# Kernel optimization log

Hardware: AMD Instinct MI355X
Metric: run time of the kernel (lower is better)

Reference implementation:

```python
import jax, jax.numpy as jnp
import numpy as np

N = 10000
E = 160000
DIMS = [512, 512, 512, 256]  # in -> hidden -> hidden -> out (num_layers=3)
EPS = 1e-12  # F.normalize default eps


def _sage_layer(x, edge_index, Wl, b, Wr):
    # PyG SAGEConv (mean aggr, normalize=True):
    # out = lin_l(mean_{j in N(i)} x_j) + lin_r(x_i), then L2-normalize rows.
    src = edge_index[0]
    dst = edge_index[1]
    msg = x[src]  # [E, d] gather of source-node features
    agg = jax.ops.segment_sum(msg, dst, num_segments=N)  # [N, d]
    cnt = jax.ops.segment_sum(jnp.ones((E,), x.dtype), dst, num_segments=N)
    mean = agg / jnp.maximum(cnt, 1.0)[:, None]
    out = mean @ Wl.T + b + x @ Wr.T
    norm = jnp.sqrt(jnp.sum(out * out, axis=-1, keepdims=True))
    return out / jnp.maximum(norm, EPS)


def setup_inputs() -> dict:
    key = jax.random.key(0)
    ks = jax.random.split(key, 2 + 3 * len(DIMS))
    x = jax.random.normal(ks[0], (N, DIMS[0]), dtype=jnp.float32)
    edge_index = jax.random.randint(ks[1], (2, E), 0, N, dtype=jnp.int64)
    inp = {"x": x, "edge_index": edge_index}
    k = 2
    for i in range(len(DIMS) - 1):
        din, dout = DIMS[i], DIMS[i + 1]
        s = 1.0 / np.sqrt(din)
        inp[f"Wl{i}"] = jax.random.uniform(ks[k], (dout, din), jnp.float32, -s, s); k += 1
        inp[f"b{i}"] = jax.random.uniform(ks[k], (dout,), jnp.float32, -s, s); k += 1
        inp[f"Wr{i}"] = jax.random.uniform(ks[k], (dout, din), jnp.float32, -s, s); k += 1
    return inp


def reference(x, edge_index, Wl0, b0, Wr0, Wl1, b1, Wr1, Wl2, b2, Wr2):
    params = [(Wl0, b0, Wr0), (Wl1, b1, Wr1), (Wl2, b2, Wr2)]
    for Wl, b, Wr in params:
        x = _sage_layer(x, edge_index, Wl, b, Wr)
        x = jax.nn.relu(x)
        # F.dropout(training=False) is identity at inference
    return x
```

## Files before the change

kernel.cpp:

```cpp
#include <hip/hip_runtime.h>

#define NN 10000

typedef __attribute__((ext_vector_type(8))) short short8;
typedef __attribute__((ext_vector_type(4))) float f32x4;

__device__ __forceinline__ ushort f2b(float f) {
    union { float f; uint32_t u; } v; v.f = f;
    uint32_t u = v.u;
    return (ushort)((u + 0x7fffu + ((u >> 16) & 1u)) >> 16);
}
__device__ __forceinline__ uint packbf(float a, float b) {
    return (uint)f2b(a) | ((uint)f2b(b) << 16);
}
__device__ __forceinline__ float blo(uint u) {
    union { uint u; float f; } v; v.u = u << 16; return v.f;
}
__device__ __forceinline__ float bhi(uint u) {
    union { uint u; float f; } v; v.u = u & 0xffff0000u; return v.f;
}

__global__ __launch_bounds__(256) void zero_int(int* __restrict__ p, int n) {
    int i = blockIdx.x * 256 + threadIdx.x;
    if (i < n) p[i] = 0;
}

__global__ __launch_bounds__(256) void count_dst(const int* __restrict__ dst,
                                                 int* __restrict__ counts, int E) {
    int i = blockIdx.x * 256 + threadIdx.x;
    if (i < E) atomicAdd(&counts[dst[i]], 1);
}

__global__ __launch_bounds__(1024) void scan_build(const int* __restrict__ counts,
                                                   int* __restrict__ offsets,
                                                   int* __restrict__ cursor,
                                                   float* __restrict__ inv_cnt, int n) {
    __shared__ int part[1024];
    int tid = threadIdx.x;
    int per = (n + 1023) / 1024;
    int base = tid * per;
    int s = 0;
    for (int i = 0; i < per; i++) { int idx = base + i; if (idx < n) s += counts[idx]; }
    part[tid] = s;
    __syncthreads();
    for (int off = 1; off < 1024; off <<= 1) {
        int v = (tid >= off) ? part[tid - off] : 0;
        __syncthreads();
        part[tid] += v;
        __syncthreads();
    }
    int run = (tid > 0) ? part[tid - 1] : 0;
    for (int i = 0; i < per; i++) {
        int idx = base + i;
        if (idx < n) {
            int c = counts[idx];
            offsets[idx] = run;
            cursor[idx]  = run;
            inv_cnt[idx] = 1.0f / fmaxf((float)c, 1.0f);
            run += c;
        }
    }
}

__global__ __launch_bounds__(256) void scatter_edges(const int* __restrict__ src,
                                                     const int* __restrict__ dst,
                                                     int* __restrict__ cursor,
                                                     int* __restrict__ sorted_src, int E) {
    int i = blockIdx.x * 256 + threadIdx.x;
    if (i < E) {
        int p = atomicAdd(&cursor[dst[i]], 1);
        sorted_src[p] = src[i];
    }
}

__global__ __launch_bounds__(256) void cvt_x(const float* __restrict__ in,
                                             ushort* __restrict__ xcat, int n4) {
    int i = blockIdx.x * 256 + threadIdx.x;
    if (i >= n4) return;
    int idx = i * 4;
    int node = idx >> 9;
    int col  = idx & 511;
    float4 v = *(const float4*)(in + (size_t)node * 512 + col);
    uint2 p;
    p.x = packbf(v.x, v.y);
    p.y = packbf(v.z, v.w);
    *(uint2*)(xcat + (size_t)node * 1024 + 512 + col) = p;
}

__global__ __launch_bounds__(256) void cvt_w(const float* __restrict__ Wl,
                                             const float* __restrict__ Wr,
                                             ushort* __restrict__ out, int n4) {
    int i = blockIdx.x * 256 + threadIdx.x;
    if (i >= n4) return;
    int idx = i * 4;
    int row = idx >> 10;
    int col = idx & 1023;
    const float* src = (col < 512) ? (Wl + (size_t)row * 512 + col)
                                   : (Wr + (size_t)row * 512 + col - 512);
    float4 v = *(const float4*)src;
    uint2 p;
    p.x = packbf(v.x, v.y);
    p.y = packbf(v.z, v.w);
    *(uint2*)(out + idx) = p;
}

__global__ __launch_bounds__(256) void agg_mean(ushort* __restrict__ xcat,
                                                const int* __restrict__ offsets,
                                                const int* __restrict__ counts,
                                                const int* __restrict__ sorted_src,
                                                const float* __restrict__ inv_cnt, int n) {
    int wave = threadIdx.x >> 6;
    int lane = threadIdx.x & 63;
    int node = blockIdx.x * 4 + wave;
    if (node >= n) return;
    int start = offsets[node];
    int cnt   = counts[node];
    float inv = inv_cnt[node];

    const uint* xr = (const uint*)xcat + 256;
    int l4 = lane * 4;

    float acc[8];
#pragma unroll
    for (int k = 0; k < 8; k++) acc[k] = 0.f;

    int e = 0;
    for (; e + 4 <= cnt; e += 4) {
        int s0 = sorted_src[start + e + 0];
        int s1 = sorted_src[start + e + 1];
        int s2 = sorted_src[start + e + 2];
        int s3 = sorted_src[start + e + 3];
        uint4 v0 = *(const uint4*)(xr + (size_t)s0 * 512 + l4);
        uint4 v1 = *(const uint4*)(xr + (size_t)s1 * 512 + l4);
        uint4 v2 = *(const uint4*)(xr + (size_t)s2 * 512 + l4);
        uint4 v3 = *(const uint4*)(xr + (size_t)s3 * 512 + l4);
#define ACC8(v) do { \
        acc[0] += blo(v.x); acc[1] += bhi(v.x); \
        acc[2] += blo(v.y); acc[3] += bhi(v.y); \
        acc[4] += blo(v.z); acc[5] += bhi(v.z); \
        acc[6] += blo(v.w); acc[7] += bhi(v.w); } while (0)
        ACC8(v0); ACC8(v1); ACC8(v2); ACC8(v3);
    }
    for (; e < cnt; e++) {
        int s0 = sorted_src[start + e];
        uint4 v0 = *(const uint4*)(xr + (size_t)s0 * 512 + l4);
        ACC8(v0);
    }
#undef ACC8

    uint4 o;
    o.x = packbf(acc[0] * inv, acc[1] * inv);
    o.y = packbf(acc[2] * inv, acc[3] * inv);
    o.z = packbf(acc[4] * inv, acc[5] * inv);
    o.w = packbf(acc[6] * inv, acc[7] * inv);
    *(uint4*)(xcat + (size_t)node * 1024 + lane * 8) = o;
}

__global__ __launch_bounds__(256) void gemm_mfma(const ushort* __restrict__ A,
                                                 const ushort* __restrict__ B,
                                                 float* __restrict__ C,
                                                 int M, int Nn) {
    __shared__ ushort Asl[64 * 32];
    __shared__ ushort Bsl[128 * 32];
    const int tid  = threadIdx.x;
    const int w    = tid >> 6;
    const int lane = tid & 63;
    const int bm = blockIdx.y * 64, bn = blockIdx.x * 128;
    const int wm = (w & 1) * 32, wn = (w >> 1) * 64;
    const int row16 = lane & 15, q = lane >> 4;

    f32x4 acc[2][4];
#pragma unroll
    for (int i = 0; i < 2; i++)
#pragma unroll
        for (int j = 0; j < 4; j++) acc[i][j] = (f32x4){0.f, 0.f, 0.f, 0.f};

    const int sc_r = lane >> 2;
    const int sc_s = lane & 3;
    const int koff = sc_s ^ ((sc_r >> 1) & 3);
    const int swz  = (row16 >> 1) & 3;

    for (int k0 = 0; k0 < 1024; k0 += 32) {
        {
            int rloc = w * 16 + sc_r;
            int grow = bm + rloc; grow = grow < M ? grow : M - 1;
            const ushort* gp = A + (size_t)grow * 1024 + k0 + koff * 8;
            __builtin_amdgcn_global_load_lds(
                (const __attribute__((address_space(1))) uint32_t*)gp,
                (__attribute__((address_space(3))) uint32_t*)&Asl[w * 512],
                16, 0, 0);
        }
#pragma unroll
        for (int c = 0; c < 2; c++) {
            int chunk = w * 2 + c;
            int rloc  = chunk * 16 + sc_r;
            const ushort* gp = B + (size_t)(bn + rloc) * 1024 + k0 + koff * 8;
            __builtin_amdgcn_global_load_lds(
                (const __attribute__((address_space(1))) uint32_t*)gp,
                (__attribute__((address_space(3))) uint32_t*)&Bsl[chunk * 512],
                16, 0, 0);
        }
        __syncthreads();

        short8 af[2], bfr[4];
        int s = q ^ swz;
#pragma unroll
        for (int i = 0; i < 2; i++) {
            int r = wm + i * 16 + row16;
            af[i] = *(const short8*)&Asl[r * 32 + s * 8];
        }
#pragma unroll
        for (int j = 0; j < 4; j++) {
            int rn = wn + j * 16 + row16;
            bfr[j] = *(const short8*)&Bsl[rn * 32 + s * 8];
        }
#pragma unroll
        for (int i = 0; i < 2; i++)
#pragma unroll
            for (int j = 0; j < 4; j++)
                acc[i][j] = __builtin_amdgcn_mfma_f32_16x16x32_bf16(
                    af[i], bfr[j], acc[i][j], 0, 0, 0);
        __syncthreads();
    }

#pragma unroll
    for (int i = 0; i < 2; i++) {
#pragma unroll
        for (int r2 = 0; r2 < 4; r2++) {
            int row = bm + wm + i * 16 + q * 4 + r2;
            if (row < M) {
                float* Cp = C + (size_t)row * Nn + bn + wn + row16;
#pragma unroll
                for (int j = 0; j < 4; j++)
                    Cp[j * 16] = acc[i][j][r2];
            }
        }
    }
}

template <int DOUT, bool FINAL>
__global__ __launch_bounds__(256) void finalize(const float* __restrict__ Cbuf,
                                                const float* __restrict__ bias,
                                                ushort* __restrict__ xcat,
                                                float* __restrict__ outf, int n) {
    const int PL = DOUT / 64;
    int wave = threadIdx.x >> 6;
    int lane = threadIdx.x & 63;
    int node = blockIdx.x * 4 + wave;
    if (node >= n) return;

    float v[PL];
    const float* Cp = Cbuf + (size_t)node * DOUT + lane * PL;
    const float* Bp = bias + lane * PL;
#pragma unroll
    for (int k = 0; k < PL; k += 4) {
        float4 c = *(const float4*)(Cp + k);
        float4 b = *(const float4*)(Bp + k);
        v[k + 0] = c.x + b.x; v[k + 1] = c.y + b.y;
        v[k + 2] = c.z + b.z; v[k + 3] = c.w + b.w;
    }
    float ss = 0.f;
#pragma unroll
    for (int k = 0; k < PL; k++) ss += v[k] * v[k];
#pragma unroll
    for (int m = 32; m >= 1; m >>= 1) ss += __shfl_xor(ss, m, 64);
    float scale = 1.0f / fmaxf(sqrtf(ss), 1e-12f);

    if (FINAL) {
        float* Op = outf + (size_t)node * DOUT + lane * PL;
#pragma unroll
        for (int k = 0; k < PL; k += 4) {
            float4 o;
            o.x = fmaxf(v[k + 0] * scale, 0.f);
            o.y = fmaxf(v[k + 1] * scale, 0.f);
            o.z = fmaxf(v[k + 2] * scale, 0.f);
            o.w = fmaxf(v[k + 3] * scale, 0.f);
            *(float4*)(Op + k) = o;
        }
    } else {
        uint4 o;
        float r0 = fmaxf(v[0] * scale, 0.f), r1 = fmaxf(v[1] * scale, 0.f);
        float r2 = fmaxf(v[2] * scale, 0.f), r3 = fmaxf(v[3] * scale, 0.f);
        float r4 = fmaxf(v[4] * scale, 0.f), r5 = fmaxf(v[5] * scale, 0.f);
        float r6 = fmaxf(v[6] * scale, 0.f), r7 = fmaxf(v[7] * scale, 0.f);
        o.x = packbf(r0, r1); o.y = packbf(r2, r3);
        o.z = packbf(r4, r5); o.w = packbf(r6, r7);
        *(uint4*)(xcat + (size_t)node * 1024 + 512 + lane * 8) = o;
    }
}

extern "C" void kernel_launch(void* const* d_in, const int* in_sizes, int n_in,
                              void* d_out, int out_size, void* d_ws, size_t ws_size,
                              hipStream_t stream) {
    const float* x    = (const float*)d_in[0];
    const int*   edge = (const int*)d_in[1];
    const float* Wl0  = (const float*)d_in[2];
    const float* b0   = (const float*)d_in[3];
    const float* Wr0  = (const float*)d_in[4];
    const float* Wl1  = (const float*)d_in[5];
    const float* b1   = (const float*)d_in[6];
    const float* Wr1  = (const float*)d_in[7];
    const float* Wl2  = (const float*)d_in[8];
    const float* b2   = (const float*)d_in[9];
    const float* Wr2  = (const float*)d_in[10];

    const int E = in_sizes[1] / 2;

    char* ws = (char*)d_ws;
    int*    counts  = (int*)(ws + 0);
    int*    offsets = (int*)(ws + 40960);
    int*    cursor  = (int*)(ws + 81920);
    float*  invc    = (float*)(ws + 122880);
    int*    sorted  = (int*)(ws + 163840);
    ushort* Wc0     = (ushort*)(ws + 804864);
    ushort* Wc1     = (ushort*)(ws + 1853440);
    ushort* Wc2     = (ushort*)(ws + 2902016);
    ushort* xcat    = (ushort*)(ws + 3426304);
    float*  Cbuf    = (float*)(ws + 23906304);

    zero_int<<<(NN + 255) / 256, 256, 0, stream>>>(counts, NN);
    count_dst<<<(E + 255) / 256, 256, 0, stream>>>(edge + E, counts, E);
    scan_build<<<1, 1024, 0, stream>>>(counts, offsets, cursor, invc, NN);
    scatter_edges<<<(E + 255) / 256, 256, 0, stream>>>(edge, edge + E, cursor, sorted, E);

    cvt_x<<<(NN * 512 / 4 + 255) / 256, 256, 0, stream>>>(x, xcat, NN * 512 / 4);
    cvt_w<<<(512 * 1024 / 4 + 255) / 256, 256, 0, stream>>>(Wl0, Wr0, Wc0, 512 * 1024 / 4);
    cvt_w<<<(512 * 1024 / 4 + 255) / 256, 256, 0, stream>>>(Wl1, Wr1, Wc1, 512 * 1024 / 4);
    cvt_w<<<(256 * 1024 / 4 + 255) / 256, 256, 0, stream>>>(Wl2, Wr2, Wc2, 256 * 1024 / 4);

    const int gyM = (NN + 63) / 64;
    const int gb  = (NN + 3) / 4;

    agg_mean<<<gb, 256, 0, stream>>>(xcat, offsets, counts, sorted, invc, NN);
    gemm_mfma<<<dim3(4, gyM), 256, 0, stream>>>(xcat, Wc0, Cbuf, NN, 512);
    finalize<512, false><<<gb, 256, 0, stream>>>(Cbuf, b0, xcat, nullptr, NN);
    agg_mean<<<gb, 256, 0, stream>>>(xcat, offsets, counts, sorted, invc, NN);
    gemm_mfma<<<dim3(4, gyM), 256, 0, stream>>>(xcat, Wc1, Cbuf, NN, 512);
    finalize<512, false><<<gb, 256, 0, stream>>>(Cbuf, b1, xcat, nullptr, NN);
    agg_mean<<<gb, 256, 0, stream>>>(xcat, offsets, counts, sorted, invc, NN);
    gemm_mfma<<<dim3(2, gyM), 256, 0, stream>>>(xcat, Wc2, Cbuf, NN, 256);
    finalize<256, true><<<gb, 256, 0, stream>>>(Cbuf, b2, nullptr, (float*)d_out, NN);
}
```

Measured before the change: 276.6 us.

## Fuse bias and row sum-of-squares into GEMM epilogue, store bf16 output

The GEMM epilogue now adds the bias, writes the result as bf16 instead of fp32, and accumulates each row's sum of squares into a buffer with a shuffle reduction plus atomicAdd. The old finalize kernel becomes a light apply_scale pass that only reads bf16 and the precomputed norm. This halves intermediate traffic and removes the per-row reduction pass. Other changes: agg_mean zeroes that buffer and unrolls its gather loop to 8 edges for more loads in flight, and the three weight-conversion launches are merged into one. The cost is rounding before normalization and float atomics, which make the reduction order nondeterministic.

```diff
diff --git a/kernel.cpp b/kernel.cpp
--- a/kernel.cpp
+++ b/kernel.cpp
@@ -87,16 +87,24 @@
     *(uint2*)(xcat + (size_t)node * 1024 + 512 + col) = p;
 }
 
-__global__ __launch_bounds__(256) void cvt_w(const float* __restrict__ Wl,
-                                             const float* __restrict__ Wr,
-                                             ushort* __restrict__ out, int n4) {
+__global__ __launch_bounds__(256) void cvt_w_all(const float* __restrict__ Wl0,
+                                                 const float* __restrict__ Wr0,
+                                                 const float* __restrict__ Wl1,
+                                                 const float* __restrict__ Wr1,
+                                                 const float* __restrict__ Wl2,
+                                                 const float* __restrict__ Wr2,
+                                                 ushort* __restrict__ out, int n4) {
     int i = blockIdx.x * 256 + threadIdx.x;
     if (i >= n4) return;
     int idx = i * 4;
     int row = idx >> 10;
     int col = idx & 1023;
-    const float* src = (col < 512) ? (Wl + (size_t)row * 512 + col)
-                                   : (Wr + (size_t)row * 512 + col - 512);
+    const float* Wl; const float* Wr; int r;
+    if (row < 512)       { Wl = Wl0; Wr = Wr0; r = row; }
+    else if (row < 1024) { Wl = Wl1; Wr = Wr1; r = row - 512; }
+    else                 { Wl = Wl2; Wr = Wr2; r = row - 1024; }
+    const float* src = (col < 512) ? (Wl + (size_t)r * 512 + col)
+                                   : (Wr + (size_t)r * 512 + col - 512);
     float4 v = *(const float4*)src;
     uint2 p;
     p.x = packbf(v.x, v.y);
@@ -108,7 +116,12 @@
                                                 const int* __restrict__ offsets,
                                                 const int* __restrict__ counts,
                                                 const int* __restrict__ sorted_src,
-                                                const float* __restrict__ inv_cnt, int n) {
+                                                const float* __restrict__ inv_cnt,
+                                                float* __restrict__ rowss, int n) {
+    if (threadIdx.x < 16) {
+        int z = blockIdx.x * 16 + (int)threadIdx.x;
+        if (z < n) rowss[z] = 0.f;
+    }
     int wave = threadIdx.x >> 6;
     int lane = threadIdx.x & 63;
     int node = blockIdx.x * 4 + wave;
@@ -124,22 +137,22 @@
 #pragma unroll
     for (int k = 0; k < 8; k++) acc[k] = 0.f;
 
+#define ACC8(v) do { \
+    acc[0] += blo(v.x); acc[1] += bhi(v.x); \
+    acc[2] += blo(v.y); acc[3] += bhi(v.y); \
+    acc[4] += blo(v.z); acc[5] += bhi(v.z); \
+    acc[6] += blo(v.w); acc[7] += bhi(v.w); } while (0)
+
     int e = 0;
-    for (; e + 4 <= cnt; e += 4) {
-        int s0 = sorted_src[start + e + 0];
-        int s1 = sorted_src[start + e + 1];
-        int s2 = sorted_src[start + e + 2];
-        int s3 = sorted_src[start + e + 3];
-        uint4 v0 = *(const uint4*)(xr + (size_t)s0 * 512 + l4);
-        uint4 v1 = *(const uint4*)(xr + (size_t)s1 * 512 + l4);
-        uint4 v2 = *(const uint4*)(xr + (size_t)s2 * 512 + l4);
-        uint4 v3 = *(const uint4*)(xr + (size_t)s3 * 512 + l4);
-#define ACC8(v) do { \
-        acc[0] += blo(v.x); acc[1] += bhi(v.x); \
-        acc[2] += blo(v.y); acc[3] += bhi(v.y); \
-        acc[4] += blo(v.z); acc[5] += bhi(v.z); \
-        acc[6] += blo(v.w); acc[7] += bhi(v.w); } while (0)
-        ACC8(v0); ACC8(v1); ACC8(v2); ACC8(v3);
+    for (; e + 8 <= cnt; e += 8) {
+        int s[8];
+#pragma unroll
+        for (int u = 0; u < 8; u++) s[u] = sorted_src[start + e + u];
+        uint4 v[8];
+#pragma unroll
+        for (int u = 0; u < 8; u++) v[u] = *(const uint4*)(xr + (size_t)s[u] * 512 + l4);
+#pragma unroll
+        for (int u = 0; u < 8; u++) ACC8(v[u]);
     }
     for (; e < cnt; e++) {
         int s0 = sorted_src[start + e];
@@ -158,7 +171,9 @@
 
 __global__ __launch_bounds__(256) void gemm_mfma(const ushort* __restrict__ A,
                                                  const ushort* __restrict__ B,
-                                                 float* __restrict__ C,
+                                                 const float* __restrict__ bias,
+                                                 ushort* __restrict__ Cb,
+                                                 float* __restrict__ rowss,
                                                  int M, int Nn) {
     __shared__ ushort Asl[64 * 32];
     __shared__ ushort Bsl[128 * 32];
@@ -223,69 +238,65 @@
         __syncthreads();
     }
 
+    float bias_v[4];
+#pragma unroll
+    for (int j = 0; j < 4; j++) bias_v[j] = bias[bn + wn + row16 + j * 16];
+
 #pragma unroll
     for (int i = 0; i < 2; i++) {
 #pragma unroll
         for (int r2 = 0; r2 < 4; r2++) {
             int row = bm + wm + i * 16 + q * 4 + r2;
+            float v0 = acc[i][0][r2] + bias_v[0];
+            float v1 = acc[i][1][r2] + bias_v[1];
+            float v2 = acc[i][2][r2] + bias_v[2];
+            float v3 = acc[i][3][r2] + bias_v[3];
+            float ssp = v0 * v0 + v1 * v1 + v2 * v2 + v3 * v3;
+            ssp += __shfl_xor(ssp, 1, 64);
+            ssp += __shfl_xor(ssp, 2, 64);
+            ssp += __shfl_xor(ssp, 4, 64);
+            ssp += __shfl_xor(ssp, 8, 64);
             if (row < M) {
-                float* Cp = C + (size_t)row * Nn + bn + wn + row16;
-#pragma unroll
-                for (int j = 0; j < 4; j++)
-                    Cp[j * 16] = acc[i][j][r2];
+                ushort* Cp = Cb + (size_t)row * Nn + bn + wn + row16;
+                Cp[0]  = f2b(v0);
+                Cp[16] = f2b(v1);
+                Cp[32] = f2b(v2);
+                Cp[48] = f2b(v3);
+                if (row16 == 0) atomicAdd(&rowss[row], ssp);
             }
         }
     }
 }
 
 template <int DOUT, bool FINAL>
-__global__ __launch_bounds__(256) void finalize(const float* __restrict__ Cbuf,
-                                                const float* __restrict__ bias,
-                                                ushort* __restrict__ xcat,
-                                                float* __restrict__ outf, int n) {
-    const int PL = DOUT / 64;
+__global__ __launch_bounds__(256) void apply_scale(const ushort* __restrict__ Cb,
+                                                   const float* __restrict__ rowss,
+                                                   ushort* __restrict__ xcat,
+                                                   float* __restrict__ outf, int n) {
     int wave = threadIdx.x >> 6;
     int lane = threadIdx.x & 63;
     int node = blockIdx.x * 4 + wave;
     if (node >= n) return;
-
-    float v[PL];
-    const float* Cp = Cbuf + (size_t)node * DOUT + lane * PL;
-    const float* Bp = bias + lane * PL;
-#pragma unroll
-    for (int k = 0; k < PL; k += 4) {
-        float4 c = *(const float4*)(Cp + k);
-        float4 b = *(const float4*)(Bp + k);
-        v[k + 0] = c.x + b.x; v[k + 1] = c.y + b.y;
-        v[k + 2] = c.z + b.z; v[k + 3] = c.w + b.w;
-    }
-    float ss = 0.f;
-#pragma unroll
-    for (int k = 0; k < PL; k++) ss += v[k] * v[k];
-#pragma unroll
-    for (int m = 32; m >= 1; m >>= 1) ss += __shfl_xor(ss, m, 64);
-    float scale = 1.0f / fmaxf(sqrtf(ss), 1e-12f);
-
-    if (FINAL) {
-        float* Op = outf + (size_t)node * DOUT + lane * PL;
-#pragma unroll
-        for (int k = 0; k < PL; k += 4) {
-            float4 o;
-            o.x = fmaxf(v[k + 0] * scale, 0.f);
-            o.y = fmaxf(v[k + 1] * scale, 0.f);
-            o.z = fmaxf(v[k + 2] * scale, 0.f);
-            o.w = fmaxf(v[k + 3] * scale, 0.f);
-            *(float4*)(Op + k) = o;
-        }
-    } else {
+    float scale = 1.0f / fmaxf(sqrtf(rowss[node]), 1e-12f);
+
+    if (DOUT == 512) {
+        uint4 v = *(const uint4*)(Cb + (size_t)node * 512 + lane * 8);
+        float r0 = fmaxf(blo(v.x) * scale, 0.f), r1 = fmaxf(bhi(v.x) * scale, 0.f);
+        float r2 = fmaxf(blo(v.y) * scale, 0.f), r3 = fmaxf(bhi(v.y) * scale, 0.f);
+        float r4 = fmaxf(blo(v.z) * scale, 0.f), r5 = fmaxf(bhi(v.z) * scale, 0.f);
+        float r6 = fmaxf(blo(v.w) * scale, 0.f), r7 = fmaxf(bhi(v.w) * scale, 0.f);
         uint4 o;
-        float r0 = fmaxf(v[0] * scale, 0.f), r1 = fmaxf(v[1] * scale, 0.f);
-        float r2 = fmaxf(v[2] * scale, 0.f), r3 = fmaxf(v[3] * scale, 0.f);
-        float r4 = fmaxf(v[4] * scale, 0.f), r5 = fmaxf(v[5] * scale, 0.f);
-        float r6 = fmaxf(v[6] * scale, 0.f), r7 = fmaxf(v[7] * scale, 0.f);
         o.x = packbf(r0, r1); o.y = packbf(r2, r3);
         o.z = packbf(r4, r5); o.w = packbf(r6, r7);
         *(uint4*)(xcat + (size_t)node * 1024 + 512 + lane * 8) = o;
+    } else {
+        uint2 v = *(const uint2*)(Cb + (size_t)node * 256 + lane * 4);
+        float4 o;
+        o.x = fmaxf(blo(v.x) * scale, 0.f);
+        o.y = fmaxf(bhi(v.x) * scale, 0.f);
+        o.z = fmaxf(blo(v.y) * scale, 0.f);
+        o.w = fmaxf(bhi(v.y) * scale, 0.f);
+        *(float4*)(outf + (size_t)node * 256 + lane * 4) = o;
     }
 }
 
@@ -312,11 +323,14 @@
     int*    cursor  = (int*)(ws + 81920);
     float*  invc    = (float*)(ws + 122880);
     int*    sorted  = (int*)(ws + 163840);
-    ushort* Wc0     = (ushort*)(ws + 804864);
-    ushort* Wc1     = (ushort*)(ws + 1853440);
-    ushort* Wc2     = (ushort*)(ws + 2902016);
+    ushort* Wcat    = (ushort*)(ws + 804864);
     ushort* xcat    = (ushort*)(ws + 3426304);
-    float*  Cbuf    = (float*)(ws + 23906304);
+    ushort* Cb      = (ushort*)(ws + 23906304);
+    float*  rowss   = (float*)(ws + 34146304);
+
+    ushort* Wc0 = Wcat;
+    ushort* Wc1 = Wcat + 512 * 1024;
+    ushort* Wc2 = Wcat + 1024 * 1024;
 
     zero_int<<<(NN + 255) / 256, 256, 0, stream>>>(counts, NN);
     count_dst<<<(E + 255) / 256, 256, 0, stream>>>(edge + E, counts, E);
@@ -324,20 +338,19 @@
     scatter_edges<<<(E + 255) / 256, 256, 0, stream>>>(edge, edge + E, cursor, sorted, E);
 
     cvt_x<<<(NN * 512 / 4 + 255) / 256, 256, 0, stream>>>(x, xcat, NN * 512 / 4);
-    cvt_w<<<(512 * 1024 / 4 + 255) / 256, 256, 0, stream>>>(Wl0, Wr0, Wc0, 512 * 1024 / 4);
-    cvt_w<<<(512 * 1024 / 4 + 255) / 256, 256, 0, stream>>>(Wl1, Wr1, Wc1, 512 * 1024 / 4);
-    cvt_w<<<(256 * 1024 / 4 + 255) / 256, 256, 0, stream>>>(Wl2, Wr2, Wc2, 256 * 1024 / 4);
+    cvt_w_all<<<(1280 * 1024 / 4 + 255) / 256, 256, 0, stream>>>(
+        Wl0, Wr0, Wl1, Wr1, Wl2, Wr2, Wcat, 1280 * 1024 / 4);
 
     const int gyM = (NN + 63) / 64;
     const int gb  = (NN + 3) / 4;
 
-    agg_mean<<<gb, 256, 0, stream>>>(xcat, offsets, counts, sorted, invc, NN);
-    gemm_mfma<<<dim3(4, gyM), 256, 0, stream>>>(xcat, Wc0, Cbuf, NN, 512);
-    finalize<512, false><<<gb, 256, 0, stream>>>(Cbuf, b0, xcat, nullptr, NN);
-    agg_mean<<<gb, 256, 0, stream>>>(xcat, offsets, counts, sorted, invc, NN);
-    gemm_mfma<<<dim3(4, gyM), 256, 0, stream>>>(xcat, Wc1, Cbuf, NN, 512);
-    finalize<512, false><<<gb, 256, 0, stream>>>(Cbuf, b1, xcat, nullptr, NN);
-    agg_mean<<<gb, 256, 0, stream>>>(xcat, offsets, counts, sorted, invc, NN);
-    gemm_mfma<<<dim3(2, gyM), 256, 0, stream>>>(xcat, Wc2, Cbuf, NN, 256);
-    finalize<256, true><<<gb, 256, 0, stream>>>(Cbuf, b2, nullptr, (float*)d_out, NN);
-}
+    agg_mean<<<gb, 256, 0, stream>>>(xcat, offsets, counts, sorted, invc, rowss, NN);
+    gemm_mfma<<<dim3(4, gyM), 256, 0, stream>>>(xcat, Wc0, b0, Cb, rowss, NN, 512);
+    apply_scale<512, false><<<gb, 256, 0, stream>>>(Cb, rowss, xcat, nullptr, NN);
+    agg_mean<<<gb, 256, 0, stream>>>(xcat, offsets, counts, sorted, invc, rowss, NN);
+    gemm_mfma<<<dim3(4, gyM), 256, 0, stream>>>(xcat, Wc1, b1, Cb, rowss, NN, 512);
+    apply_scale<512, false><<<gb, 256, 0, stream>>>(Cb, rowss, xcat, nullptr, NN);
+    agg_mean<<<gb, 256, 0, stream>>>(xcat, offsets, counts, sorted, invc, rowss, NN);
+    gemm_mfma<<<dim3(2, gyM), 256, 0, stream>>>(xcat, Wc2, b2, Cb, rowss, NN, 256);
+    apply_scale<256, true><<<gb, 256, 0, stream>>>(Cb, rowss, nullptr, (float*)d_out, NN);
+}
```

New measurement: 280.5 us. Within noise of the previous version (+1.4%).

## Shard neighbor aggregation by feature chunk and fuse setup kernels

Applied to the files above, without the earlier changes.

The mean aggregation now splits each node's 512 features into 8 chunks handled by separate blocks, with 16 lanes per node and 8 edges unrolled per step. The aim is more memory-level parallelism and a smaller per-block gather footprint, so that chunked neighbor rows may stay resident in cache. Separately, count zeroing is folded into cvt_x, edge counting into a single merged weight-conversion kernel, and the three weight conversions are merged into one launch to cut launch overhead. The risks are narrower 8-byte gathers, and that counting inside cvt_w_all depends on cvt_x having zeroed counts earlier on the same stream.

```diff
diff --git a/kernel.cpp b/kernel.cpp
--- a/kernel.cpp
+++ b/kernel.cpp
@@ -18,17 +18,6 @@
 }
 __device__ __forceinline__ float bhi(uint u) {
     union { uint u; float f; } v; v.u = u & 0xffff0000u; return v.f;
-}
-
-__global__ __launch_bounds__(256) void zero_int(int* __restrict__ p, int n) {
-    int i = blockIdx.x * 256 + threadIdx.x;
-    if (i < n) p[i] = 0;
-}
-
-__global__ __launch_bounds__(256) void count_dst(const int* __restrict__ dst,
-                                                 int* __restrict__ counts, int E) {
-    int i = blockIdx.x * 256 + threadIdx.x;
-    if (i < E) atomicAdd(&counts[dst[i]], 1);
 }
 
 __global__ __launch_bounds__(1024) void scan_build(const int* __restrict__ counts,
@@ -74,8 +63,10 @@
 }
 
 __global__ __launch_bounds__(256) void cvt_x(const float* __restrict__ in,
-                                             ushort* __restrict__ xcat, int n4) {
+                                             ushort* __restrict__ xcat,
+                                             int* __restrict__ counts, int n4) {
     int i = blockIdx.x * 256 + threadIdx.x;
+    if (i < NN) counts[i] = 0;
     if (i >= n4) return;
     int idx = i * 4;
     int node = idx >> 9;
@@ -87,16 +78,28 @@
     *(uint2*)(xcat + (size_t)node * 1024 + 512 + col) = p;
 }
 
-__global__ __launch_bounds__(256) void cvt_w(const float* __restrict__ Wl,
-                                             const float* __restrict__ Wr,
-                                             ushort* __restrict__ out, int n4) {
+__global__ __launch_bounds__(256) void cvt_w_all(const float* __restrict__ Wl0,
+                                                 const float* __restrict__ Wr0,
+                                                 const float* __restrict__ Wl1,
+                                                 const float* __restrict__ Wr1,
+                                                 const float* __restrict__ Wl2,
+                                                 const float* __restrict__ Wr2,
+                                                 ushort* __restrict__ out,
+                                                 const int* __restrict__ dst,
+                                                 int* __restrict__ counts,
+                                                 int E, int n4) {
     int i = blockIdx.x * 256 + threadIdx.x;
+    if (i < E) atomicAdd(&counts[dst[i]], 1);
     if (i >= n4) return;
     int idx = i * 4;
     int row = idx >> 10;
     int col = idx & 1023;
-    const float* src = (col < 512) ? (Wl + (size_t)row * 512 + col)
-                                   : (Wr + (size_t)row * 512 + col - 512);
+    const float* Wl; const float* Wr; int r;
+    if (row < 512)       { Wl = Wl0; Wr = Wr0; r = row; }
+    else if (row < 1024) { Wl = Wl1; Wr = Wr1; r = row - 512; }
+    else                 { Wl = Wl2; Wr = Wr2; r = row - 1024; }
+    const float* src = (col < 512) ? (Wl + (size_t)r * 512 + col)
+                                   : (Wr + (size_t)r * 512 + col - 512);
     float4 v = *(const float4*)src;
     uint2 p;
     p.x = packbf(v.x, v.y);
@@ -104,56 +107,54 @@
     *(uint2*)(out + idx) = p;
 }
 
-__global__ __launch_bounds__(256) void agg_mean(ushort* __restrict__ xcat,
-                                                const int* __restrict__ offsets,
-                                                const int* __restrict__ counts,
-                                                const int* __restrict__ sorted_src,
-                                                const float* __restrict__ inv_cnt, int n) {
-    int wave = threadIdx.x >> 6;
-    int lane = threadIdx.x & 63;
-    int node = blockIdx.x * 4 + wave;
+__global__ __launch_bounds__(256) void agg_shard(ushort* __restrict__ xcat,
+                                                 const int* __restrict__ offsets,
+                                                 const int* __restrict__ counts,
+                                                 const int* __restrict__ sorted_src,
+                                                 const float* __restrict__ inv_cnt, int n) {
+    int chunk = blockIdx.x & 7;
+    int nb    = blockIdx.x >> 3;
+    int wave  = threadIdx.x >> 6;
+    int lane  = threadIdx.x & 63;
+    int sub   = lane >> 4;
+    int l16   = lane & 15;
+    int node  = nb * 16 + wave * 4 + sub;
     if (node >= n) return;
     int start = offsets[node];
     int cnt   = counts[node];
     float inv = inv_cnt[node];
 
-    const uint* xr = (const uint*)xcat + 256;
-    int l4 = lane * 4;
-
-    float acc[8];
-#pragma unroll
-    for (int k = 0; k < 8; k++) acc[k] = 0.f;
+    const uint* xr = (const uint*)xcat;
+    int cu = 256 + chunk * 32 + l16 * 2;
+
+    float a0 = 0.f, a1 = 0.f, a2 = 0.f, a3 = 0.f;
+
+#define ACC4(v) do { \
+    a0 += blo(v.x); a1 += bhi(v.x); \
+    a2 += blo(v.y); a3 += bhi(v.y); } while (0)
 
     int e = 0;
-    for (; e + 4 <= cnt; e += 4) {
-        int s0 = sorted_src[start + e + 0];
-        int s1 = sorted_src[start + e + 1];
-        int s2 = sorted_src[start + e + 2];
-        int s3 = sorted_src[start + e + 3];
-        uint4 v0 = *(const uint4*)(xr + (size_t)s0 * 512 + l4);
-        uint4 v1 = *(const uint4*)(xr + (size_t)s1 * 512 + l4);
-        uint4 v2 = *(const uint4*)(xr + (size_t)s2 * 512 + l4);
-        uint4 v3 = *(const uint4*)(xr + (size_t)s3 * 512 + l4);
-#define ACC8(v) do { \
-        acc[0] += blo(v.x); acc[1] += bhi(v.x); \
-        acc[2] += blo(v.y); acc[3] += bhi(v.y); \
-        acc[4] += blo(v.z); acc[5] += bhi(v.z); \
-        acc[6] += blo(v.w); acc[7] += bhi(v.w); } while (0)
-        ACC8(v0); ACC8(v1); ACC8(v2); ACC8(v3);
+    for (; e + 8 <= cnt; e += 8) {
+        int s[8];
+#pragma unroll
+        for (int u = 0; u < 8; u++) s[u] = sorted_src[start + e + u];
+        uint2 v[8];
+#pragma unroll
+        for (int u = 0; u < 8; u++) v[u] = *(const uint2*)(xr + (size_t)s[u] * 512 + cu);
+#pragma unroll
+        for (int u = 0; u < 8; u++) ACC4(v[u]);
     }
     for (; e < cnt; e++) {
         int s0 = sorted_src[start + e];
-        uint4 v0 = *(const uint4*)(xr + (size_t)s0 * 512 + l4);
-        ACC8(v0);
-    }
-#undef ACC8
-
-    uint4 o;
-    o.x = packbf(acc[0] * inv, acc[1] * inv);
-    o.y = packbf(acc[2] * inv, acc[3] * inv);
-    o.z = packbf(acc[4] * inv, acc[5] * inv);
-    o.w = packbf(acc[6] * inv, acc[7] * inv);
-    *(uint4*)(xcat + (size_t)node * 1024 + lane * 8) = o;
+        uint2 v0 = *(const uint2*)(xr + (size_t)s0 * 512 + cu);
+        ACC4(v0);
+    }
+#undef ACC4
+
+    uint2 o;
+    o.x = packbf(a0 * inv, a1 * inv);
+    o.y = packbf(a2 * inv, a3 * inv);
+    *(uint2*)(xcat + (size_t)node * 1024 + chunk * 64 + l16 * 4) = o;
 }
 
 __global__ __launch_bounds__(256) void gemm_mfma(const ushort* __restrict__ A,
@@ -312,32 +313,31 @@
     int*    cursor  = (int*)(ws + 81920);
     float*  invc    = (float*)(ws + 122880);
     int*    sorted  = (int*)(ws + 163840);
-    ushort* Wc0     = (ushort*)(ws + 804864);
-    ushort* Wc1     = (ushort*)(ws + 1853440);
-    ushort* Wc2     = (ushort*)(ws + 2902016);
+    ushort* Wcat    = (ushort*)(ws + 804864);
     ushort* xcat    = (ushort*)(ws + 3426304);
     float*  Cbuf    = (float*)(ws + 23906304);
 
-    zero_int<<<(NN + 255) / 256, 256, 0, stream>>>(counts, NN);
-    count_dst<<<(E + 255) / 256, 256, 0, stream>>>(edge + E, counts, E);
+    ushort* Wc0 = Wcat;
+    ushort* Wc1 = Wcat + 512 * 1024;
+    ushort* Wc2 = Wcat + 1024 * 1024;
+
+    cvt_x<<<(NN * 512 / 4 + 255) / 256, 256, 0, stream>>>(x, xcat, counts, NN * 512 / 4);
+    cvt_w_all<<<(1280 * 1024 / 4 + 255) / 256, 256, 0, stream>>>(
+        Wl0, Wr0, Wl1, Wr1, Wl2, Wr2, Wcat, edge + E, counts, E, 1280 * 1024 / 4);
     scan_build<<<1, 1024, 0, stream>>>(counts, offsets, cursor, invc, NN);
     scatter_edges<<<(E + 255) / 256, 256, 0, stream>>>(edge, edge + E, cursor, sorted, E);
 
-    cvt_x<<<(NN * 512 / 4 + 255) / 256, 256, 0, stream>>>(x, xcat, NN * 512 / 4);
-    cvt_w<<<(512 * 1024 / 4 + 255) / 256, 256, 0, stream>>>(Wl0, Wr0, Wc0, 512 * 1024 / 4);
-    cvt_w<<<(512 * 1024 / 4 + 255) / 256, 256, 0, stream>>>(Wl1, Wr1, Wc1, 512 * 1024 / 4);
-    cvt_w<<<(256 * 1024 / 4 + 255) / 256, 256, 0, stream>>>(Wl2, Wr2, Wc2, 256 * 1024 / 4);
-
     const int gyM = (NN + 63) / 64;
+    const int gAgg = 8 * ((NN + 15) / 16);
     const int gb  = (NN + 3) / 4;
 
-    agg_mean<<<gb, 256, 0, stream>>>(xcat, offsets, counts, sorted, invc, NN);
+    agg_shard<<<gAgg, 256, 0, stream>>>(xcat, offsets, counts, sorted, invc, NN);
     gemm_mfma<<<dim3(4, gyM), 256, 0, stream>>>(xcat, Wc0, Cbuf, NN, 512);
     finalize<512, false><<<gb, 256, 0, stream>>>(Cbuf, b0, xcat, nullptr, NN);
-    agg_mean<<<gb, 256, 0, stream>>>(xcat, offsets, counts, sorted, invc, NN);
+    agg_shard<<<gAgg, 256, 0, stream>>>(xcat, offsets, counts, sorted, invc, NN);
     gemm_mfma<<<dim3(4, gyM), 256, 0, stream>>>(xcat, Wc1, Cbuf, NN, 512);
     finalize<512, false><<<gb, 256, 0, stream>>>(Cbuf, b1, xcat, nullptr, NN);
-    agg_mean<<<gb, 256, 0, stream>>>(xcat, offsets, counts, sorted, invc, NN);
+    agg_shard<<<gAgg, 256, 0, stream>>>(xcat, offsets, counts, sorted, invc, NN);
     gemm_mfma<<<dim3(2, gyM), 256, 0, stream>>>(xcat, Wc2, Cbuf, NN, 256);
     finalize<256, true><<<gb, 256, 0, stream>>>(Cbuf, b2, nullptr, (float*)d_out, NN);
 }
```

Result: no change. 281.2 us (+1.7%).
